# Kernel optimization log

Measured on AMD Instinct MI355X. Metric: run time of the kernel, lower is better.

## Reference

```python
import jax, jax.numpy as jnp
import numpy as np

B, S, DQ, DK, H, D = 4, 2048, 1024, 1024, 16, 64


def setup_inputs() -> dict:
    key = jax.random.key(0)
    k1, k2, k3, k4 = jax.random.split(key, 4)
    # xavier_uniform bound for Linear(in, out): sqrt(6/(in+out))
    bq = float(np.sqrt(6.0 / (DQ + H * D)))
    bk = float(np.sqrt(6.0 / (DK + H * D)))
    return {
        "query_input": jax.random.normal(k1, (B, S, DQ), dtype=jnp.float32),
        "key_input": jax.random.normal(k2, (B, S, DK), dtype=jnp.float32),
        "Wq": jax.random.uniform(k3, (H * D, DQ), minval=-bq, maxval=bq, dtype=jnp.float32),
        "bq": jnp.zeros((H * D,), dtype=jnp.float32),
        "Wk": jax.random.uniform(k4, (H * D, DK), minval=-bk, maxval=bk, dtype=jnp.float32),
        "bk": jnp.zeros((H * D,), dtype=jnp.float32),
    }


def reference(query_input, key_input, Wq, bq, Wk, bk):
    scaling = D ** (-0.5)
    # projections: (B, S, H*D) -> (B, S, H, D)
    q = (query_input @ Wq.T + bq).reshape(B, S, H, D) * scaling
    k = (key_input @ Wk.T + bk).reshape(B, S, H, D)
    # scores: (B, H, S, S), softmax over keys
    scores = jnp.einsum("bqhd,bkhd->bhqk", q, k)
    attn = jax.nn.softmax(scores, axis=-1)
    # NOTE: module reuses K as the value tensor (no V projection)
    out = jnp.einsum("bhqk,bkhd->bqhd", attn, k)
    return out.reshape(B, S, H * D)
```

## Files before the change

kernel.cpp:

```cpp
#include <hip/hip_runtime.h>
#include <stdint.h>

#define NB 4
#define NS 2048
#define NH 16
#define ND 64
#define NHD 1024
#define NK 1024

typedef __attribute__((ext_vector_type(8))) short short8;
typedef __attribute__((ext_vector_type(4))) float f32x4;
typedef __attribute__((ext_vector_type(16))) float f32x16;
typedef __attribute__((ext_vector_type(4))) unsigned u32x4;

__device__ __forceinline__ unsigned short f2bf(float f) {
    union { float f; unsigned u; } v; v.f = f;
    return (unsigned short)((v.u + 0x7fffu + ((v.u >> 16) & 1u)) >> 16);
}

__device__ __forceinline__ void gload_lds16(const unsigned short* g, unsigned short* l) {
    __builtin_amdgcn_global_load_lds(
        (const __attribute__((address_space(1))) void*)g,
        (__attribute__((address_space(3))) void*)l, 16, 0, 0);
}

__device__ __forceinline__ unsigned cvtpk(float lo, float hi) {
    unsigned r;
    asm volatile("v_cvt_pk_bf16_f32 %0, %1, %2" : "=v"(r) : "v"(lo), "v"(hi));
    return r;
}
__device__ __forceinline__ void plswap(unsigned& a, unsigned& b) {
    asm volatile("v_permlane32_swap_b32 %0, %1" : "+v"(a), "+v"(b));
}
__device__ __forceinline__ float exp2_raw(float x) {
    float r;
    asm("v_exp_f32 %0, %1" : "=v"(r) : "v"(x));
    return r;
}

__global__ void cvt_w_bf16(const float* __restrict__ Wq, const float* __restrict__ Wk,
                           unsigned short* __restrict__ Wqb, unsigned short* __restrict__ Wkb) {
    const int n4 = (NK * NHD) / 4;
    const int stride = gridDim.x * blockDim.x;
    for (int i = blockIdx.x * blockDim.x + threadIdx.x; i < 2 * n4; i += stride) {
        const int m = i < n4 ? 0 : 1;
        const int j = m ? i - n4 : i;
        const float4 v = m ? ((const float4*)Wk)[j] : ((const float4*)Wq)[j];
        ushort4 o;
        o.x = f2bf(v.x); o.y = f2bf(v.y); o.z = f2bf(v.z); o.w = f2bf(v.w);
        if (m) ((ushort4*)Wkb)[j] = o; else ((ushort4*)Wqb)[j] = o;
    }
}

#define PH_SYNC() do { __builtin_amdgcn_s_barrier(); __builtin_amdgcn_sched_barrier(0); \
    asm volatile("s_waitcnt lgkmcnt(0)" ::: "memory"); __builtin_amdgcn_sched_barrier(0); } while (0)
#define PH_END()  do { __builtin_amdgcn_s_barrier(); __builtin_amdgcn_sched_barrier(0); } while (0)

#define RD_AF(MH, KK)                                                                     \
    _Pragma("unroll")                                                                     \
    for (int mi_ = 0; mi_ < 4; ++mi_) {                                                   \
        const int rowA_ = wm + (MH) * 64 + mi_ * 16 + lr;                                 \
        af[mi_] = *(const short8*)(Ab + (rowA_ << 7) + (((KK) * 64 + lg * 16) ^ swzr));   \
    }
#define RD_BF(KK)                                                                         \
    _Pragma("unroll")                                                                     \
    for (int ni_ = 0; ni_ < 4; ++ni_) {                                                   \
        const int rowB_ = wn + ni_ * 16 + lr;                                             \
        bfr[ni_] = *(const short8*)(Bb + (rowB_ << 7) + (((KK) * 64 + lg * 16) ^ swzr));  \
    }
#define DO_MFMA(MH)                                                                       \
    do {                                                                                  \
        __builtin_amdgcn_s_setprio(1);                                                    \
        _Pragma("unroll")                                                                 \
        for (int mi_ = 0; mi_ < 4; ++mi_)                                                 \
            _Pragma("unroll")                                                             \
            for (int ni_ = 0; ni_ < 4; ++ni_)                                             \
                acc[(MH) * 4 + mi_][ni_] = __builtin_amdgcn_mfma_f32_16x16x32_bf16(       \
                    af[mi_], bfr[ni_], acc[(MH) * 4 + mi_][ni_], 0, 0, 0);                \
        __builtin_amdgcn_s_setprio(0);                                                    \
    } while (0)

__global__ __launch_bounds__(512, 2) void proj_gemm3(
    const float* __restrict__ Xq,
    const float* __restrict__ Xk,
    const unsigned short* __restrict__ Wqb,
    const unsigned short* __restrict__ Wkb,
    const float* __restrict__ bqv,
    const float* __restrict__ bkv,
    unsigned short* __restrict__ Qo,
    unsigned short* __restrict__ Ko,
    unsigned short* __restrict__ KTo,
    float qscale)
{
    extern __shared__ __attribute__((aligned(16))) char smem[];

    const int bid = blockIdx.x;
    const int wg = (bid & 7) * 32 + (bid >> 3);
    const int mp = wg >> 2;
    const int nb = wg & 3;
    const int which = mp >> 5;
    const long bm = (long)(mp & 31) * 256;
    const long bn = (long)nb * 256;

    const float* A32         = which ? Xk : Xq;
    const unsigned short* Wt = which ? Wkb : Wqb;
    const float* bias        = which ? bkv : bqv;
    unsigned short* outp     = which ? Ko : Qo;
    unsigned short* outT     = which ? KTo : nullptr;
    const float scale        = which ? 1.0f : qscale;

    const int t = threadIdx.x;
    const int lane = t & 63;
    const int w = t >> 6;
    const int wm = (w >> 2) * 128, wn = (w & 3) * 64;
    const int lr = lane & 15, lg = lane >> 4;
    const int swzr = (lr & 7) << 4;

    f32x4 acc[8][4];
    #pragma unroll
    for (int i = 0; i < 8; ++i)
        #pragma unroll
        for (int jj = 0; jj < 4; ++jj) acc[i][jj] = (f32x4){0.f, 0.f, 0.f, 0.f};

    float4 aset[8];

    auto LOADA = [&](int k0) {
        #pragma unroll
        for (int c = 0; c < 4; ++c) {
            const int u2 = c * 512 + t;
            const int row = u2 >> 3, c8 = u2 & 7;
            const float* src = A32 + (bm + row) * (long)NK + k0 + c8 * 8;
            aset[2 * c]     = *(const float4*)src;
            aset[2 * c + 1] = *(const float4*)(src + 4);
        }
    };
    auto WRITEA = [&](int buf) {
        char* Ad = smem + buf * 32768;
        #pragma unroll
        for (int c = 0; c < 4; ++c) {
            const int u2 = c * 512 + t;
            const int row = u2 >> 3;
            const int cbyte = ((u2 & 7) << 4) ^ ((row & 7) << 4);
            u32x4 wv;
            wv[0] = cvtpk(aset[2 * c].x, aset[2 * c].y);
            wv[1] = cvtpk(aset[2 * c].z, aset[2 * c].w);
            wv[2] = cvtpk(aset[2 * c + 1].x, aset[2 * c + 1].y);
            wv[3] = cvtpk(aset[2 * c + 1].z, aset[2 * c + 1].w);
            *(u32x4*)(Ad + (row << 7) + cbyte) = wv;
        }
    };
    const int scolB = (((lane & 7) ^ (lane >> 3)) << 3);
    auto BGLOAD = [&](int k0, int buf) {
        unsigned short* Bd = (unsigned short*)(smem + 65536 + buf * 32768);
        #pragma unroll
        for (int c = 0; c < 4; ++c) {
            const int rowB = c * 64 + w * 8 + (lane >> 3);
            gload_lds16(Wt + (bn + rowB) * (long)NK + k0 + scolB,
                        Bd + (size_t)(c * 64 + w * 8) * 64);
        }
    };

    BGLOAD(0, 0);
    asm volatile("" ::: "memory");
    LOADA(0);
    asm volatile("" ::: "memory");
    WRITEA(0);
    __builtin_amdgcn_sched_barrier(0);
    LOADA(64);
    asm volatile("s_waitcnt lgkmcnt(0)" ::: "memory");
    __builtin_amdgcn_s_barrier();
    __builtin_amdgcn_sched_barrier(0);

    for (int it = 0; it < 16; ++it) {
        const int cur = it & 1;
        const char* Ab = (const char*)smem + cur * 32768;
        const char* Bb = (const char*)smem + 65536 + cur * 32768;
        short8 af[4], bfr[4];

        RD_BF(0); RD_AF(0, 0);
        if (it + 1 < 16) BGLOAD((it + 1) * 64, cur ^ 1);
        PH_SYNC(); DO_MFMA(0); PH_END();

        RD_AF(1, 0);
        if (it + 1 < 16) WRITEA(cur ^ 1);
        PH_SYNC(); DO_MFMA(1); PH_END();

        RD_BF(1); RD_AF(0, 1);
        if (it + 2 < 16) LOADA((it + 2) * 64);
        PH_SYNC(); DO_MFMA(0); PH_END();

        RD_AF(1, 1);
        if (it + 2 < 16)      asm volatile("s_waitcnt vmcnt(8)" ::: "memory");
        else if (it + 1 < 16) asm volatile("s_waitcnt vmcnt(0)" ::: "memory");
        PH_SYNC(); DO_MFMA(1); PH_END();
    }

    #pragma unroll
    for (int ni = 0; ni < 4; ++ni) {
        const int n = (int)bn + wn + ni * 16 + lr;
        const float bv = bias[n];
        const int h = n >> 6, d = n & 63;
        #pragma unroll
        for (int mi = 0; mi < 8; ++mi) {
            const int m0 = (int)bm + wm + mi * 16 + lg * 4;
            const int b = m0 >> 11, s0 = m0 & 2047;
            unsigned short vv[4];
            #pragma unroll
            for (int r = 0; r < 4; ++r) {
                const float v = (acc[mi][ni][r] + bv) * scale;
                vv[r] = f2bf(v);
                outp[(((size_t)(b * NH + h)) * NS + (s0 + r)) * ND + d] = vv[r];
            }
            if (outT) {
                ushort4 tv; tv.x = vv[0]; tv.y = vv[1]; tv.z = vv[2]; tv.w = vv[3];
                *(ushort4*)&outT[(((size_t)(b * NH + h)) * ND + d) * NS + s0] = tv;
            }
        }
    }
}

#define PACK_P(s0, s1, paw, lsum)                                              \
    do {                                                                       \
        _Pragma("unroll")                                                      \
        for (int tt_ = 0; tt_ < 2; ++tt_) {                                    \
            unsigned c_[8];                                                    \
            _Pragma("unroll")                                                  \
            for (int j_ = 0; j_ < 8; ++j_) {                                   \
                const float plo_ = exp2_raw(tt_ ? s1[2 * j_]     : s0[2 * j_]);   \
                const float phi_ = exp2_raw(tt_ ? s1[2 * j_ + 1] : s0[2 * j_ + 1]); \
                (lsum) += plo_ + phi_;                                         \
                c_[j_] = cvtpk(plo_, phi_);                                    \
            }                                                                  \
            plswap(c_[0], c_[2]); plswap(c_[1], c_[3]);                        \
            plswap(c_[4], c_[6]); plswap(c_[5], c_[7]);                        \
            paw[2 * tt_]     = (u32x4){c_[0], c_[1], c_[2], c_[3]};            \
            paw[2 * tt_ + 1] = (u32x4){c_[4], c_[5], c_[6], c_[7]};            \
        }                                                                      \
    } while (0)

__global__ __launch_bounds__(512, 4) void attn_fused(
    const unsigned short* __restrict__ Qb,
    const unsigned short* __restrict__ Kb,
    const unsigned short* __restrict__ KTb,
    float* __restrict__ outp)
{
    __shared__ __attribute__((aligned(16))) unsigned short LDSA[2 * 4 * 4096];

    const int t = threadIdx.x;
    const int lane = t & 63;
    const int wq = t >> 6;
    const int q5 = lane & 31;
    const int hi = lane >> 5;

    const int Bid = blockIdx.x + 8 * blockIdx.y + 128 * blockIdx.z;
    const int xcd = Bid & 7;
    const int wIdx = Bid >> 3;
    const int qblk = wIdx & 7;
    const int g = xcd * 8 + (wIdx >> 3);
    const int h = g & 15, b = g >> 4;
    const int qbase = qblk * 256 + wq * 32;

    const unsigned short* Qh  = Qb  + ((size_t)(b * NH + h)) * NS * ND;
    const unsigned short* Kh  = Kb  + ((size_t)(b * NH + h)) * NS * ND;
    const unsigned short* KTh = KTb + ((size_t)(b * NH + h)) * ND * NS;

    short8 qB[4];
    {
        const unsigned short* Qrow = Qh + (size_t)(qbase + q5) * ND;
        #pragma unroll
        for (int kd = 0; kd < 4; ++kd)
            qB[kd] = *(const short8*)&Qrow[kd * 16 + hi * 8];
    }

    const int srow = wq * 8 + (lane >> 3);
    const int scol = ((((lane & 7) << 4) ^ ((srow & 7) << 4)) >> 1);

    f32x16 acc0, acc1;
    float l_run = 0.f;
    #pragma unroll
    for (int r = 0; r < 16; ++r) { acc0[r] = 0.f; acc1[r] = 0.f; }

    const int swz = (q5 & 7) << 4;
    const int ro0 = q5 * 128, ro1 = ro0 + 4096;

    auto STAGE = [&](int buf, int kt ) {
        unsigned short* Bd = &LDSA[buf * 16384];
        gload_lds16(Kh  + (size_t)(kt + srow) * ND + scol,        Bd         + wq * 512);
        gload_lds16(KTh + (size_t)srow * NS + kt + scol,          Bd + 4096  + wq * 512);
        gload_lds16(Kh  + (size_t)(kt + 64 + srow) * ND + scol,   Bd + 8192  + wq * 512);
        gload_lds16(KTh + (size_t)srow * NS + (kt + 64) + scol,   Bd + 12288 + wq * 512);
    };

    auto COMPUTE = [&](const char* Kbuf) {
        const char* Ktbuf = Kbuf + 8192;

        f32x16 s0, s1;
        #pragma unroll
        for (int r = 0; r < 16; ++r) { s0[r] = 0.f; s1[r] = 0.f; }
        __builtin_amdgcn_s_setprio(1);
        #pragma unroll
        for (int kd = 0; kd < 4; ++kd) {
            const int cb = (kd * 32 + hi * 16) ^ swz;
            short8 kf0 = *(const short8*)(Kbuf + ro0 + cb);
            short8 kf1 = *(const short8*)(Kbuf + ro1 + cb);
            s0 = __builtin_amdgcn_mfma_f32_32x32x16_bf16(kf0, qB[kd], s0, 0, 0, 0);
            s1 = __builtin_amdgcn_mfma_f32_32x32x16_bf16(kf1, qB[kd], s1, 0, 0, 0);
        }
        __builtin_amdgcn_s_setprio(0);

        u32x4 paw[4];
        PACK_P(s0, s1, paw, l_run);

        __builtin_amdgcn_s_setprio(1);
        #pragma unroll
        for (int ks = 0; ks < 4; ++ks) {
            union { u32x4 u; short8 s; } pa; pa.u = paw[ks];
            const int cb = (ks * 32 + hi * 16) ^ swz;
            short8 vf0 = *(const short8*)(Ktbuf + ro0 + cb);
            short8 vf1 = *(const short8*)(Ktbuf + ro1 + cb);
            acc0 = __builtin_amdgcn_mfma_f32_32x32x16_bf16(pa.s, vf0, acc0, 0, 0, 0);
            acc1 = __builtin_amdgcn_mfma_f32_32x32x16_bf16(pa.s, vf1, acc1, 0, 0, 0);
        }
        __builtin_amdgcn_s_setprio(0);
    };

    STAGE(0, 0);
    for (int it = 0; it < NS / 128; ++it) {
        const int cur = it & 1;
        asm volatile("s_waitcnt vmcnt(0)" ::: "memory");
        __syncthreads();
        if (it < NS / 128 - 1) STAGE(cur ^ 1, (it + 1) * 128);

        const char* base = (const char*)LDSA + cur * 32768;
        COMPUTE(base);
        COMPUTE(base + 16384);
    }

    const float lt = l_run + __shfl_xor(l_run, 32);
    const float inv = 1.0f / lt;
    #pragma unroll
    for (int r = 0; r < 16; ++r) {
        const int qr = (r & 3) + 8 * (r >> 2) + 4 * hi;
        const float invr = __shfl(inv, qr);
        float* orow = outp + ((size_t)b * NS + (qbase + qr)) * NHD + h * ND;
        orow[q5]      = acc0[r] * invr;
        orow[32 + q5] = acc1[r] * invr;
    }
}

extern "C" void kernel_launch(void* const* d_in, const int* in_sizes, int n_in,
                              void* d_out, int out_size, void* d_ws, size_t ws_size,
                              hipStream_t stream) {
    const float* xq = (const float*)d_in[0];
    const float* xk = (const float*)d_in[1];
    const float* Wq = (const float*)d_in[2];
    const float* bq = (const float*)d_in[3];
    const float* Wk = (const float*)d_in[4];
    const float* bk = (const float*)d_in[5];
    float* outp = (float*)d_out;

    unsigned short* Wqb = (unsigned short*)d_ws;
    unsigned short* Wkb = Wqb + 1048576;
    unsigned short* Qb  = Wkb + 1048576;
    unsigned short* Kb  = Qb  + 8388608;
    unsigned short* KTb = Kb  + 8388608;

    static bool lds_init = false;
    if (!lds_init) {
        hipFuncSetAttribute((const void*)proj_gemm3,
                            hipFuncAttributeMaxDynamicSharedMemorySize, 131072);
        lds_init = true;
    }

    cvt_w_bf16<<<1024, 256, 0, stream>>>(Wq, Wk, Wqb, Wkb);

    const float qscale = 0.125f * 1.4426950408889634f;
    proj_gemm3<<<256, 512, 131072, stream>>>(xq, xk, Wqb, Wkb, bq, bk,
                                             Qb, Kb, KTb, qscale);

    attn_fused<<<dim3(8, 16, 4), 512, 0, stream>>>(Qb, Kb, KTb, outp);
}
```

Baseline: 142.1 us.

## Pre-convert activations to bf16 and load projection A tiles via global_load_lds

Moves the fp32-to-bf16 conversion of the query and key activations out of the projection GEMM into the standalone conversion kernel, which now also handles the weights. The GEMM then fetches A tiles straight into LDS with global_load_lds, the same way it already fetches B, so register staging and in-loop conversion go away. The cost is an extra full read and write of the activations (about 32 MB read, 16 MB written) in a separate kernel, more workspace, and a simpler prefetch that now waits on vmcnt(0) every iteration.

```diff
diff --git a/kernel.cpp b/kernel.cpp
--- a/kernel.cpp
+++ b/kernel.cpp
@@ -38,17 +38,26 @@
     return r;
 }
 
-__global__ void cvt_w_bf16(const float* __restrict__ Wq, const float* __restrict__ Wk,
-                           unsigned short* __restrict__ Wqb, unsigned short* __restrict__ Wkb) {
-    const int n4 = (NK * NHD) / 4;
+__global__ void cvt_all_bf16(const float* __restrict__ Wq, const float* __restrict__ Wk,
+                             const float* __restrict__ Xq, const float* __restrict__ Xk,
+                             unsigned short* __restrict__ Wqb, unsigned short* __restrict__ Wkb,
+                             unsigned short* __restrict__ Xqb, unsigned short* __restrict__ Xkb) {
+    const int w4 = (NK * NHD) / 4;
+    const int x4 = (NB * NS * NK) / 4;
+    const int total = 2 * w4 + 2 * x4;
     const int stride = gridDim.x * blockDim.x;
-    for (int i = blockIdx.x * blockDim.x + threadIdx.x; i < 2 * n4; i += stride) {
-        const int m = i < n4 ? 0 : 1;
-        const int j = m ? i - n4 : i;
-        const float4 v = m ? ((const float4*)Wk)[j] : ((const float4*)Wq)[j];
+    for (int i = blockIdx.x * blockDim.x + threadIdx.x; i < total; i += stride) {
+        const float4* src;
+        ushort4* dst;
+        int j;
+        if (i < w4)                { j = i;                src = (const float4*)Wq; dst = (ushort4*)Wqb; }
+        else if (i < 2 * w4)       { j = i - w4;           src = (const float4*)Wk; dst = (ushort4*)Wkb; }
+        else if (i < 2 * w4 + x4)  { j = i - 2 * w4;       src = (const float4*)Xq; dst = (ushort4*)Xqb; }
+        else                       { j = i - 2 * w4 - x4;  src = (const float4*)Xk; dst = (ushort4*)Xkb; }
+        const float4 v = src[j];
         ushort4 o;
         o.x = f2bf(v.x); o.y = f2bf(v.y); o.z = f2bf(v.z); o.w = f2bf(v.w);
-        if (m) ((ushort4*)Wkb)[j] = o; else ((ushort4*)Wqb)[j] = o;
+        dst[j] = o;
     }
 }
 
@@ -80,9 +89,9 @@
         __builtin_amdgcn_s_setprio(0);                                                    \
     } while (0)
 
-__global__ __launch_bounds__(512, 2) void proj_gemm3(
-    const float* __restrict__ Xq,
-    const float* __restrict__ Xk,
+__global__ __launch_bounds__(512, 2) void proj_gemm4(
+    const unsigned short* __restrict__ Xqb,
+    const unsigned short* __restrict__ Xkb,
     const unsigned short* __restrict__ Wqb,
     const unsigned short* __restrict__ Wkb,
     const float* __restrict__ bqv,
@@ -102,7 +111,7 @@
     const long bm = (long)(mp & 31) * 256;
     const long bn = (long)nb * 256;
 
-    const float* A32         = which ? Xk : Xq;
+    const unsigned short* Xb = which ? Xkb : Xqb;
     const unsigned short* Wt = which ? Wkb : Wqb;
     const float* bias        = which ? bkv : bqv;
     unsigned short* outp     = which ? Ko : Qo;
@@ -122,33 +131,6 @@
         #pragma unroll
         for (int jj = 0; jj < 4; ++jj) acc[i][jj] = (f32x4){0.f, 0.f, 0.f, 0.f};
 
-    float4 aset[8];
-
-    auto LOADA = [&](int k0) {
-        #pragma unroll
-        for (int c = 0; c < 4; ++c) {
-            const int u2 = c * 512 + t;
-            const int row = u2 >> 3, c8 = u2 & 7;
-            const float* src = A32 + (bm + row) * (long)NK + k0 + c8 * 8;
-            aset[2 * c]     = *(const float4*)src;
-            aset[2 * c + 1] = *(const float4*)(src + 4);
-        }
-    };
-    auto WRITEA = [&](int buf) {
-        char* Ad = smem + buf * 32768;
-        #pragma unroll
-        for (int c = 0; c < 4; ++c) {
-            const int u2 = c * 512 + t;
-            const int row = u2 >> 3;
-            const int cbyte = ((u2 & 7) << 4) ^ ((row & 7) << 4);
-            u32x4 wv;
-            wv[0] = cvtpk(aset[2 * c].x, aset[2 * c].y);
-            wv[1] = cvtpk(aset[2 * c].z, aset[2 * c].w);
-            wv[2] = cvtpk(aset[2 * c + 1].x, aset[2 * c + 1].y);
-            wv[3] = cvtpk(aset[2 * c + 1].z, aset[2 * c + 1].w);
-            *(u32x4*)(Ad + (row << 7) + cbyte) = wv;
-        }
-    };
     const int scolB = (((lane & 7) ^ (lane >> 3)) << 3);
     auto BGLOAD = [&](int k0, int buf) {
         unsigned short* Bd = (unsigned short*)(smem + 65536 + buf * 32768);
@@ -159,15 +141,19 @@
                         Bd + (size_t)(c * 64 + w * 8) * 64);
         }
     };
+    auto AGLOAD = [&](int k0, int buf) {
+        unsigned short* Ad = (unsigned short*)(smem + buf * 32768);
+        #pragma unroll
+        for (int c = 0; c < 4; ++c) {
+            const int rowA = c * 64 + w * 8 + (lane >> 3);
+            gload_lds16(Xb + (bm + rowA) * (long)NK + k0 + scolB,
+                        Ad + (size_t)(c * 64 + w * 8) * 64);
+        }
+    };
 
     BGLOAD(0, 0);
-    asm volatile("" ::: "memory");
-    LOADA(0);
-    asm volatile("" ::: "memory");
-    WRITEA(0);
-    __builtin_amdgcn_sched_barrier(0);
-    LOADA(64);
-    asm volatile("s_waitcnt lgkmcnt(0)" ::: "memory");
+    AGLOAD(0, 0);
+    asm volatile("s_waitcnt vmcnt(0)" ::: "memory");
     __builtin_amdgcn_s_barrier();
     __builtin_amdgcn_sched_barrier(0);
 
@@ -182,16 +168,14 @@
         PH_SYNC(); DO_MFMA(0); PH_END();
 
         RD_AF(1, 0);
-        if (it + 1 < 16) WRITEA(cur ^ 1);
+        if (it + 1 < 16) AGLOAD((it + 1) * 64, cur ^ 1);
         PH_SYNC(); DO_MFMA(1); PH_END();
 
         RD_BF(1); RD_AF(0, 1);
-        if (it + 2 < 16) LOADA((it + 2) * 64);
         PH_SYNC(); DO_MFMA(0); PH_END();
 
         RD_AF(1, 1);
-        if (it + 2 < 16)      asm volatile("s_waitcnt vmcnt(8)" ::: "memory");
-        else if (it + 1 < 16) asm volatile("s_waitcnt vmcnt(0)" ::: "memory");
+        if (it + 1 < 16) asm volatile("s_waitcnt vmcnt(0)" ::: "memory");
         PH_SYNC(); DO_MFMA(1); PH_END();
     }
 
@@ -364,18 +348,20 @@
     unsigned short* Qb  = Wkb + 1048576;
     unsigned short* Kb  = Qb  + 8388608;
     unsigned short* KTb = Kb  + 8388608;
+    unsigned short* Xqb = KTb + 8388608;
+    unsigned short* Xkb = Xqb + 8388608;
 
     static bool lds_init = false;
     if (!lds_init) {
-        hipFuncSetAttribute((const void*)proj_gemm3,
+        hipFuncSetAttribute((const void*)proj_gemm4,
                             hipFuncAttributeMaxDynamicSharedMemorySize, 131072);
         lds_init = true;
     }
 
-    cvt_w_bf16<<<1024, 256, 0, stream>>>(Wq, Wk, Wqb, Wkb);
+    cvt_all_bf16<<<1024, 256, 0, stream>>>(Wq, Wk, xq, xk, Wqb, Wkb, Xqb, Xkb);
 
     const float qscale = 0.125f * 1.4426950408889634f;
-    proj_gemm3<<<256, 512, 131072, stream>>>(xq, xk, Wqb, Wkb, bq, bk,
+    proj_gemm4<<<256, 512, 131072, stream>>>(Xqb, Xkb, Wqb, Wkb, bq, bk,
                                              Qb, Kb, KTb, qscale);
 
     attn_fused<<<dim3(8, 16, 4), 512, 0, stream>>>(Qb, Kb, KTb, outp);
```

After: 145.7 us. +2.6%, slower.
